# Performance work log

Hardware: AMD Instinct MI355X
Metric: run time of the kernel (lower is better)

Reference implementation:

```python
import jax, jax.numpy as jnp
import numpy as np
from jax import lax

B, N, D_FEAT = 16, 4096, 20
NPOINT, NSAMPLE = 1024, 32
MLP = [64, 64, 128]
IN_CH = 3 + 1 + D_FEAT  # grouped_xyz_norm(3) + L2 norm(1) + grouped_depth_norm(20)
BN_EPS = 1e-5


def setup_inputs() -> dict:
    key = jax.random.key(0)
    ks = jax.random.split(key, 20)
    inp = {
        "xyz": jax.random.normal(ks[0], (B, 3, N), dtype=jnp.float32),
        "feature": jax.random.normal(ks[1], (B, N, D_FEAT), dtype=jnp.float32),
    }
    last = IN_CH
    kidx = 2
    for li, out_ch in enumerate(MLP):
        inp[f"w{li}"] = jax.random.normal(ks[kidx], (out_ch, last), dtype=jnp.float32) * (1.0 / np.sqrt(last)); kidx += 1
        inp[f"b{li}"] = jax.random.normal(ks[kidx], (out_ch,), dtype=jnp.float32) * 0.01; kidx += 1
        inp[f"g{li}"] = 1.0 + 0.1 * jax.random.normal(ks[kidx], (out_ch,), dtype=jnp.float32); kidx += 1
        inp[f"bt{li}"] = 0.1 * jax.random.normal(ks[kidx], (out_ch,), dtype=jnp.float32); kidx += 1
        last = out_ch
    return inp


def square_distance(src, dst):
    # [B,S,C] x [B,M,C] -> [B,S,M]
    d = -2.0 * jnp.einsum("bsc,bmc->bsm", src, dst)
    d = d + jnp.sum(src * src, -1)[:, :, None]
    d = d + jnp.sum(dst * dst, -1)[:, None, :]
    return d


def farthest_point_sample(pts, npoint):
    # pts: [B,N,C]; deterministic start at index 0 (torch uses random start)
    b, n, _ = pts.shape
    bidx = jnp.arange(b)

    def step(carry, _):
        dist, far = carry
        centroid = pts[bidx, far]                      # [B,C]
        d = jnp.sum((pts - centroid[:, None, :]) ** 2, -1)  # [B,N]
        dist = jnp.minimum(dist, d)
        nxt = jnp.argmax(dist, -1)
        return (dist, nxt), far

    init = (jnp.full((b, n), 1e10, pts.dtype), jnp.zeros((b,), jnp.int32))
    _, idx = lax.scan(step, init, None, length=npoint)
    return idx.T  # [B,npoint]


def _gather_groups(points, idx):
    # points [B,N,C], idx [B,S,K] -> [B,S,K,C]
    return jax.vmap(lambda p, i: p[i])(points, idx)


def conv_bn_relu(x, w, b, g, bt):
    # x [B,C,K,S]; 1x1 conv = channel matmul; BN in training mode (batch stats, biased var)
    y = jnp.einsum("bcks,oc->boks", x, w) + b[None, :, None, None]
    mu = jnp.mean(y, axis=(0, 2, 3), keepdims=True)
    var = jnp.mean((y - mu) ** 2, axis=(0, 2, 3), keepdims=True)
    y = (y - mu) * lax.rsqrt(var + BN_EPS)
    y = y * g[None, :, None, None] + bt[None, :, None, None]
    return jax.nn.relu(y)


def reference(xyz, feature, w0, b0, g0, bt0, w1, b1, g1, bt1, w2, b2, g2, bt2):
    xyz_n = jnp.transpose(xyz, (0, 2, 1))              # [B,N,3]
    combined = jnp.concatenate([xyz_n, feature], -1)   # [B,N,23]
    fps_idx = farthest_point_sample(combined, NPOINT)  # [B,S]

    new_bin = jnp.take_along_axis(feature, fps_idx[:, :, None], axis=1)  # [B,S,20]
    new_xyz = jnp.take_along_axis(xyz_n, fps_idx[:, :, None], axis=1)    # [B,S,3]

    sqd = square_distance(new_bin, feature) + square_distance(new_xyz, xyz_n)  # [B,S,N]
    idx = jnp.argsort(sqd, axis=-1)[:, :, :NSAMPLE]    # [B,S,K]

    gxyz = _gather_groups(xyz_n, idx)                  # [B,S,K,3]
    gfeat = _gather_groups(feature, idx)               # [B,S,K,20]
    gxyz_norm = gxyz - new_xyz[:, :, None, :]
    gdep_norm = gfeat - new_bin[:, :, None, :]
    nrm = jnp.sqrt(jnp.maximum(jnp.sum(gxyz_norm ** 2, -1, keepdims=True), 1e-12))
    new_points = jnp.concatenate([gxyz_norm, nrm, gdep_norm], -1)  # [B,S,K,24]

    x = jnp.transpose(new_points, (0, 3, 2, 1))        # [B,24,K,S]
    for (w, b, g, bt) in [(w0, b0, g0, bt0), (w1, b1, g1, bt1), (w2, b2, g2, bt2)]:
        x = conv_bn_relu(x, w, b, g, bt)
    out = jnp.max(x, axis=2)                           # [B,128,S]
    return jnp.transpose(new_xyz, (0, 2, 1)), out, new_bin
```

## Files before the change

### kernel.cpp

```cpp
#include <hip/hip_runtime.h>

#define BB 16
#define NN 4096
#define DFEAT 20
#define SS 1024
#define KK 32
#define MM (BB*SS*KK)

#define WS_STATS   0ull
#define WS_PARAMS  8192ull
#define WS_FPSIDX  12288ull
#define WS_CENT    81920ull
#define WS_KNN     1654784ull
#define WS_COMB    3751936ull
#define WS_YB      10043392ull
#define WS_NEED    77152256ull

typedef float v2f __attribute__((ext_vector_type(2)));

static __device__ __forceinline__ unsigned short f2bf(float f){
    unsigned u = __float_as_uint(f);
    unsigned r = (u + 0x7FFFu + ((u >> 16) & 1u)) >> 16;
    return (unsigned short)r;
}
static __device__ __forceinline__ float bf2f(unsigned short v){
    return __uint_as_float((unsigned)v << 16);
}
static __device__ __forceinline__ void pinv2(v2f& x){
    asm volatile("" : "+v"(x));
}

static __device__ __forceinline__ unsigned long long max64(unsigned long long a, unsigned long long b){
    return a > b ? a : b;
}
template<int CTRL>
static __device__ __forceinline__ unsigned dpp32_or0(unsigned x){
    return (unsigned)__builtin_amdgcn_update_dpp(0, (int)x, CTRL, 0xf, 0xf, true);
}
template<int CTRL>
static __device__ __forceinline__ unsigned long long dpp_move64(unsigned long long k){
    int tlo = __builtin_amdgcn_update_dpp(0, (int)(unsigned)k,         CTRL, 0xf, 0xf, true);
    int thi = __builtin_amdgcn_update_dpp(0, (int)(unsigned)(k >> 32), CTRL, 0xf, 0xf, true);
    return ((unsigned long long)(unsigned)thi << 32) | (unsigned)tlo;
}
static __device__ __forceinline__ unsigned umax32(unsigned a, unsigned b){
    return a > b ? a : b;
}
static __device__ __forceinline__ unsigned wave_max_u32(unsigned x){
    x = umax32(x, dpp32_or0<0x111>(x));
    x = umax32(x, dpp32_or0<0x112>(x));
    x = umax32(x, dpp32_or0<0x114>(x));
    x = umax32(x, dpp32_or0<0x118>(x));
    x = umax32(x, dpp32_or0<0x142>(x));
    x = umax32(x, dpp32_or0<0x143>(x));
    return x;
}

__global__ void k_zstats(double* __restrict__ stats){
    int t = threadIdx.x;
#pragma unroll
    for (int i = 0; i < 4; ++i) stats[i*256 + t] = 0.0;
}

__global__ void k_fail(float* __restrict__ out, int n){
    int i = blockIdx.x * 256 + threadIdx.x;
    if (i < n) out[i] = 0.f;
}

__global__ __launch_bounds__(256) void k_build(const float* __restrict__ xyz,
                                               const float* __restrict__ feat,
                                               float* __restrict__ comb)
{
    int idx = blockIdx.x * 256 + threadIdx.x;
    int b = idx >> 12, j = idx & 4095;
    float c[24];
    c[0] = xyz[((size_t)b*3 + 0)*NN + j];
    c[1] = xyz[((size_t)b*3 + 1)*NN + j];
    c[2] = xyz[((size_t)b*3 + 2)*NN + j];
    const float* f = feat + ((size_t)b*NN + j)*DFEAT;
#pragma unroll
    for (int d = 0; d < 20; ++d) c[3+d] = f[d];
    c[23] = 0.f;
    float* out = comb + (size_t)idx * 24;
#pragma unroll
    for (int q = 0; q < 6; ++q)
        ((float4*)out)[q] = make_float4(c[4*q], c[4*q+1], c[4*q+2], c[4*q+3]);
}

__global__ __launch_bounds__(1024, 4) void k_fps(const float* __restrict__ comb,
                                                 int* __restrict__ fpsidx)
{
    int b = blockIdx.x, t = threadIdx.x;
    const float* C = comb + (size_t)b * NN * 24;
    v2f pt2[2][24];
    v2f dist2[2];
#pragma unroll
    for (int p = 0; p < 4; ++p){
        const float4* r = (const float4*)(C + (size_t)(t + 1024*p) * 24);
#pragma unroll
        for (int q = 0; q < 6; ++q){
            float4 v = r[q];
            pt2[p>>1][4*q+0][p&1] = v.x;
            pt2[p>>1][4*q+1][p&1] = v.y;
            pt2[p>>1][4*q+2][p&1] = v.z;
            pt2[p>>1][4*q+3][p&1] = v.w;
        }
    }
#pragma unroll
    for (int k = 0; k < 2; ++k)
        dist2[k] = (v2f){1e10f, 1e10f};

    __shared__ __align__(16) unsigned long long wkey[2][16];
    __shared__ __align__(16) float wpt[2][16][24];
    __shared__ int fps_lds[SS];
    int lane = t & 63, w = t >> 6;
    unsigned nt = 0xFFFFFFFFu - (unsigned)t;
    int far = 0;

    float cc[24];
    {
        const float4* crow = (const float4*)C;
#pragma unroll
        for (int q = 0; q < 6; ++q){
            float4 cv = crow[q];
            cc[4*q] = cv.x; cc[4*q+1] = cv.y; cc[4*q+2] = cv.z; cc[4*q+3] = cv.w;
        }
    }

    for (int s = 0; s < SS; ++s){
#pragma unroll
        for (int k = 0; k < 2; ++k)
#pragma unroll
            for (int q = 0; q < 23; ++q) pinv2(pt2[k][q]);

        if (t == 0) fps_lds[s] = far;
        v2f acc2[2];
#pragma unroll
        for (int k = 0; k < 2; ++k){
            v2f d0 = pt2[k][0] - cc[0];
            acc2[k] = d0 * d0;
        }
#pragma unroll
        for (int q = 1; q < 23; ++q){
            float cq = cc[q];
#pragma unroll
            for (int k = 0; k < 2; ++k){
                v2f dd = pt2[k][q] - cq;
                acc2[k] = __builtin_elementwise_fma(dd, dd, acc2[k]);
            }
        }
#pragma unroll
        for (int k = 0; k < 2; ++k)
            dist2[k] = __builtin_elementwise_min(dist2[k], acc2[k]);
        v2f mt = __builtin_elementwise_max(dist2[0], dist2[1]);
        float mf = fmaxf(mt[0], mt[1]);
        unsigned maxbits = __float_as_uint(mf);
        int pstar = 0;
#pragma unroll
        for (int p = 3; p >= 0; --p)
            if (__float_as_uint(dist2[p>>1][p&1]) == maxbits) pstar = p;

        unsigned M = __builtin_amdgcn_readlane((int)wave_max_u32(maxbits), 63);
        unsigned cidx = (maxbits == M) ? (nt - ((unsigned)pstar << 10)) : 0u;
        unsigned widxc = __builtin_amdgcn_readlane((int)wave_max_u32(cidx), 63);
        unsigned widx  = 0xFFFFFFFFu - widxc;

        int par = s & 1;
        if (lane == 63)
            wkey[par][w] = ((unsigned long long)M << 32) | (unsigned long long)widxc;
        if (t == (int)(widx & 1023u)){
            int pw = (int)(widx >> 10);
            float* dst = wpt[par][w];
            switch (pw){
#define PE(P,q) pt2[(P)>>1][q][(P)&1]
#define STASH(P) case P: \
                ((float4*)dst)[0] = make_float4(PE(P,0),PE(P,1),PE(P,2),PE(P,3)); \
                ((float4*)dst)[1] = make_float4(PE(P,4),PE(P,5),PE(P,6),PE(P,7)); \
                ((float4*)dst)[2] = make_float4(PE(P,8),PE(P,9),PE(P,10),PE(P,11)); \
                ((float4*)dst)[3] = make_float4(PE(P,12),PE(P,13),PE(P,14),PE(P,15)); \
                ((float4*)dst)[4] = make_float4(PE(P,16),PE(P,17),PE(P,18),PE(P,19)); \
                ((float4*)dst)[5] = make_float4(PE(P,20),PE(P,21),PE(P,22),0.f); \
                break;
            STASH(0) STASH(1) STASH(2) STASH(3)
#undef STASH
#undef PE
            }
        }
        __syncthreads();
        unsigned long long k2 = wkey[par][lane & 15];
        k2 = max64(k2, dpp_move64<0x121>(k2));
        k2 = max64(k2, dpp_move64<0x122>(k2));
        k2 = max64(k2, dpp_move64<0x124>(k2));
        k2 = max64(k2, dpp_move64<0x128>(k2));
        far = (int)(0xFFFFFFFFu - (unsigned)(k2 & 0xFFFFFFFFull));
        int wg = (far & 1023) >> 6;
        const float4* crow = (const float4*)wpt[par][wg];
#pragma unroll
        for (int q = 0; q < 6; ++q){
            float4 cv = crow[q];
            cc[4*q] = cv.x; cc[4*q+1] = cv.y; cc[4*q+2] = cv.z; cc[4*q+3] = cv.w;
        }
    }
    __syncthreads();
    fpsidx[b*SS + t] = fps_lds[t];
}

__global__ __launch_bounds__(256) void k_gather(const float* __restrict__ comb,
                                                const int* __restrict__ fpsidx,
                                                float* __restrict__ cent,
                                                float* __restrict__ out0,
                                                float* __restrict__ out2)
{
    int idx = blockIdx.x * 256 + threadIdx.x;
    int b = idx >> 10, s = idx & 1023;
    int j = fpsidx[idx];
    const float* row = comb + ((size_t)b*NN + j) * 24;
    float* cr = cent + (size_t)idx * 24;
#pragma unroll
    for (int q = 0; q < 6; ++q) ((float4*)cr)[q] = ((const float4*)row)[q];
#pragma unroll
    for (int c = 0; c < 3; ++c) out0[((size_t)b*3 + c)*SS + s] = row[c];
    float* o2 = out2 + (size_t)idx * 20;
#pragma unroll
    for (int d = 0; d < 20; ++d) o2[d] = row[3 + d];
}

__global__ __launch_bounds__(256) void k_knn(const float* __restrict__ comb,
                                             const float* __restrict__ cent,
                                             int* __restrict__ knn)
{
    int w = threadIdx.x >> 6, lane = threadIdx.x & 63;
    int r = blockIdx.x * 4 + w;
    int b = r >> 10;
    const float* crow = cent + (size_t)r * 24;
    const float* P0 = comb + (size_t)b * NN * 24;
    double cc[24];
#pragma unroll
    for (int q = 0; q < 24; ++q) cc[q] = (double)crow[q];
    unsigned u[64];
#pragma unroll
    for (int k = 0; k < 64; ++k){
        int j = k*64 + lane;
        const float4* pr = (const float4*)(P0 + (size_t)j * 24);
        double acc = 0.0;
#pragma unroll
        for (int q = 0; q < 6; ++q){
            float4 v = pr[q];
            double d0 = (double)v.x - cc[4*q];
            double d1 = (double)v.y - cc[4*q+1];
            double d2 = (double)v.z - cc[4*q+2];
            double d3 = (double)v.w - cc[4*q+3];
            acc += d0*d0; acc += d1*d1; acc += d2*d2; acc += d3*d3;
        }
        u[k] = __float_as_uint((float)acc);
    }
    unsigned lo = 0u, hi = 0xFFFFFFFFu;
    for (int it = 0; it < 32; ++it){
        unsigned mid = lo + ((hi - lo) >> 1);
        int cnt = 0;
#pragma unroll
        for (int k = 0; k < 64; ++k) cnt += (u[k] <= mid) ? 1 : 0;
#pragma unroll
        for (int off = 32; off > 0; off >>= 1) cnt += __shfl_xor(cnt, off);
        if (cnt >= KK) hi = mid; else lo = mid + 1;
    }
    unsigned T = lo;
    int* orow = knn + (size_t)r * KK;
    unsigned long long lmask = (1ull << lane) - 1ull;
    int pos = 0;
#pragma unroll
    for (int k = 0; k < 64; ++k){
        bool lt = (u[k] < T);
        unsigned long long mk = __ballot(lt);
        if (lt) orow[pos + __popcll(mk & lmask)] = k*64 + lane;
        pos += __popcll(mk);
    }
#pragma unroll
    for (int k = 0; k < 64; ++k){
        if (pos >= KK) break;
        bool eq = (u[k] == T);
        unsigned long long mk = __ballot(eq);
        int rk = __popcll(mk & lmask);
        if (eq && (pos + rk) < KK) orow[pos + rk] = k*64 + lane;
        pos += __popcll(mk);
    }
}

__global__ __launch_bounds__(256) void k_l1(const float* __restrict__ comb,
                                            const float* __restrict__ cent,
                                            const int* __restrict__ knn,
                                            const float* __restrict__ w0,
                                            const float* __restrict__ b0,
                                            unsigned short* __restrict__ yb)
{
    __shared__ float Wt[24][64];
    __shared__ float Xt[24][68];
    int t = threadIdx.x;
    int m_base = blockIdx.x * 64;
    for (int i = t; i < 1536; i += 256){
        int o = i / 24, c = i - o*24;
        Wt[c][o] = w0[i];
    }
    {
        int sm = t & 63, g = t >> 6;
        int m = m_base + sm;
        int b = m >> 15;
        int row = m >> 5;
        int j = knn[m];
        const float* P  = comb + ((size_t)b*NN + j) * 24;
        const float* Cc = cent + (size_t)row * 24;
        if (g == 0){
            float dx = P[0]-Cc[0], dy = P[1]-Cc[1], dz = P[2]-Cc[2];
            Xt[0][sm] = dx; Xt[1][sm] = dy; Xt[2][sm] = dz;
            float n2 = dx*dx; n2 = fmaf(dy, dy, n2); n2 = fmaf(dz, dz, n2);
            Xt[3][sm] = sqrtf(fmaxf(n2, 1e-12f));
            Xt[4][sm] = P[3] - Cc[3];
            Xt[5][sm] = P[4] - Cc[4];
        } else {
#pragma unroll
            for (int cq = 0; cq < 6; ++cq){
                int c = 6*g + cq;
                Xt[c][sm] = P[c-1] - Cc[c-1];
            }
        }
    }
    __syncthreads();
    int i = t >> 4, jj = t & 15;
    float acc[4][4] = {};
#pragma unroll
    for (int c = 0; c < 24; ++c){
        float4 wv = *(const float4*)&Wt[c][i*4];
        float4 xv = *(const float4*)&Xt[c][jj*4];
        float wr[4] = {wv.x, wv.y, wv.z, wv.w};
        float xr[4] = {xv.x, xv.y, xv.z, xv.w};
#pragma unroll
        for (int a = 0; a < 4; ++a)
#pragma unroll
            for (int q = 0; q < 4; ++q) acc[a][q] = fmaf(wr[a], xr[q], acc[a][q]);
    }
#pragma unroll
    for (int oi = 0; oi < 4; ++oi){
        int o = i*4 + oi;
        float bb = b0[o];
        ushort4 rv;
        rv.x = f2bf(acc[oi][0]+bb); rv.y = f2bf(acc[oi][1]+bb);
        rv.z = f2bf(acc[oi][2]+bb); rv.w = f2bf(acc[oi][3]+bb);
        *(ushort4*)&yb[(size_t)o*MM + m_base + jj*4] = rv;
    }
}

__global__ __launch_bounds__(256) void k_stats(const unsigned short* __restrict__ y,
                                               double* __restrict__ stats)
{
    const int chunks = 8;
    int c = blockIdx.x / chunks, ch = blockIdx.x % chunks;
    size_t base = (size_t)c * MM + (size_t)ch * (MM / chunks);
    double s1 = 0.0, s2 = 0.0;
    const unsigned short* p = y + base;
    for (int i = threadIdx.x; i < MM/chunks; i += 256){
        float v = bf2f(p[i]);
        s1 += v; s2 += (double)v * v;
    }
#pragma unroll
    for (int off = 32; off > 0; off >>= 1){
        s1 += __shfl_xor(s1, off);
        s2 += __shfl_xor(s2, off);
    }
    __shared__ double ps1[4], ps2[4];
    int w = threadIdx.x >> 6, lane = threadIdx.x & 63;
    if (lane == 0){ ps1[w] = s1; ps2[w] = s2; }
    __syncthreads();
    if (threadIdx.x == 0){
        atomicAdd(&stats[c*2 + 0], ps1[0]+ps1[1]+ps1[2]+ps1[3]);
        atomicAdd(&stats[c*2 + 1], ps2[0]+ps2[1]+ps2[2]+ps2[3]);
    }
}

__global__ void k_affine(const double* __restrict__ stats, float* __restrict__ params, int C)
{
    int c = threadIdx.x;
    if (c < C){
        double mu = stats[c*2] / (double)MM;
        double var = stats[c*2 + 1] / (double)MM - mu*mu;
        params[c*2 + 0] = (float)mu;
        params[c*2 + 1] = (float)(1.0 / sqrt(var + 1e-5));
    }
}

__global__ __launch_bounds__(256) void k_l2(unsigned short* __restrict__ yb,
                                            const float* __restrict__ prm,
                                            const float* __restrict__ gg,
                                            const float* __restrict__ bt,
                                            const float* __restrict__ w,
                                            const float* __restrict__ bias)
{
    __shared__ float Wt[64][64];
    __shared__ float Xt[64][68];
    int t = threadIdx.x;
    int m_base = blockIdx.x * 64;
    for (int i = t; i < 4096; i += 256){
        int o = i >> 6, c = i & 63;
        Wt[c][o] = w[i];
    }
#pragma unroll
    for (int rp = 0; rp < 16; ++rp){
        int idx = rp*256 + t;
        int c = idx >> 6, mm2 = idx & 63;
        float v = bf2f(yb[(size_t)c*MM + m_base + mm2]);
        float t1 = (v - prm[c*2]) * prm[c*2 + 1];
        Xt[c][mm2] = fmaxf(fmaf(t1, gg[c], bt[c]), 0.f);
    }
    __syncthreads();
    int i = t >> 4, jj = t & 15;
    float acc[4][4] = {};
#pragma unroll
    for (int c = 0; c < 64; ++c){
        float4 wv = *(const float4*)&Wt[c][i*4];
        float4 xv = *(const float4*)&Xt[c][jj*4];
        float wr[4] = {wv.x, wv.y, wv.z, wv.w};
        float xr[4] = {xv.x, xv.y, xv.z, xv.w};
#pragma unroll
        for (int a = 0; a < 4; ++a)
#pragma unroll
            for (int q = 0; q < 4; ++q) acc[a][q] = fmaf(wr[a], xr[q], acc[a][q]);
    }
#pragma unroll
    for (int oi = 0; oi < 4; ++oi){
        int o = i*4 + oi;
        float bb = bias[o];
        ushort4 rv;
        rv.x = f2bf(acc[oi][0]+bb); rv.y = f2bf(acc[oi][1]+bb);
        rv.z = f2bf(acc[oi][2]+bb); rv.w = f2bf(acc[oi][3]+bb);
        *(ushort4*)&yb[(size_t)o*MM + m_base + jj*4] = rv;
    }
}

__global__ __launch_bounds__(256) void k_l3s(const unsigned short* __restrict__ yb,
                                             const float* __restrict__ prm,
                                             const float* __restrict__ gg,
                                             const float* __restrict__ bt,
                                             const float* __restrict__ w,
                                             const float* __restrict__ bias,
                                             double* __restrict__ stats)
{
    __shared__ float Wt[64][128];
    __shared__ float Xt[64][68];
    int t = threadIdx.x;
    for (int i = t; i < 8192; i += 256){
        int o = i >> 6, c = i & 63;
        Wt[c][o] = w[i];
    }
    int i = t >> 4, jj = t & 15;
    double s1[8] = {}, s2[8] = {};
    for (int tt = 0; tt < 16; ++tt){
        int m_base = (blockIdx.x * 16 + tt) * 64;
        __syncthreads();
#pragma unroll
        for (int rp = 0; rp < 16; ++rp){
            int idx = rp*256 + t;
            int c = idx >> 6, mm2 = idx & 63;
            float v = bf2f(yb[(size_t)c*MM + m_base + mm2]);
            float t1 = (v - prm[c*2]) * prm[c*2 + 1];
            Xt[c][mm2] = fmaxf(fmaf(t1, gg[c], bt[c]), 0.f);
        }
        __syncthreads();
        float acc[8][4] = {};
#pragma unroll
        for (int c = 0; c < 64; ++c){
            float4 w0v = *(const float4*)&Wt[c][i*8];
            float4 w1v = *(const float4*)&Wt[c][i*8 + 4];
            float4 xv  = *(const float4*)&Xt[c][jj*4];
            float wr[8] = {w0v.x, w0v.y, w0v.z, w0v.w, w1v.x, w1v.y, w1v.z, w1v.w};
            float xr[4] = {xv.x, xv.y, xv.z, xv.w};
#pragma unroll
            for (int a = 0; a < 8; ++a)
#pragma unroll
                for (int q = 0; q < 4; ++q) acc[a][q] = fmaf(wr[a], xr[q], acc[a][q]);
        }
#pragma unroll
        for (int oi = 0; oi < 8; ++oi){
            float bb = bias[i*8 + oi];
#pragma unroll
            for (int q = 0; q < 4; ++q){
                float v = acc[oi][q] + bb;
                s1[oi] += v;
                s2[oi] += (double)v * v;
            }
        }
    }
#pragma unroll
    for (int oi = 0; oi < 8; ++oi){
#pragma unroll
        for (int off = 1; off < 16; off <<= 1){
            s1[oi] += __shfl_xor(s1[oi], off);
            s2[oi] += __shfl_xor(s2[oi], off);
        }
    }
    if (jj == 0){
#pragma unroll
        for (int oi = 0; oi < 8; ++oi){
            int o = i*8 + oi;
            atomicAdd(&stats[o*2 + 0], s1[oi]);
            atomicAdd(&stats[o*2 + 1], s2[oi]);
        }
    }
}

__global__ __launch_bounds__(256) void k_final(const unsigned short* __restrict__ yb,
                                               const float* __restrict__ prm2,
                                               const float* __restrict__ g1c,
                                               const float* __restrict__ bt1c,
                                               const float* __restrict__ w,
                                               const float* __restrict__ bias,
                                               const float* __restrict__ prm3,
                                               const float* __restrict__ g2c,
                                               const float* __restrict__ bt2c,
                                               float* __restrict__ out1)
{
    __shared__ float Wt[64][128];
    __shared__ float Xt[64][68];
    int t = threadIdx.x;
    int m_base = blockIdx.x * 64;
    for (int i = t; i < 8192; i += 256){
        int o = i >> 6, c = i & 63;
        Wt[c][o] = w[i];
    }
#pragma unroll
    for (int rp = 0; rp < 16; ++rp){
        int idx = rp*256 + t;
        int c = idx >> 6, mm2 = idx & 63;
        float v = bf2f(yb[(size_t)c*MM + m_base + mm2]);
        float t1 = (v - prm2[c*2]) * prm2[c*2 + 1];
        Xt[c][mm2] = fmaxf(fmaf(t1, g1c[c], bt1c[c]), 0.f);
    }
    __syncthreads();
    int i = t >> 4, jj = t & 15;
    float acc[8][4] = {};
#pragma unroll
    for (int c = 0; c < 64; ++c){
        float4 w0v = *(const float4*)&Wt[c][i*8];
        float4 w1v = *(const float4*)&Wt[c][i*8 + 4];
        float4 xv  = *(const float4*)&Xt[c][jj*4];
        float wr[8] = {w0v.x, w0v.y, w0v.z, w0v.w, w1v.x, w1v.y, w1v.z, w1v.w};
        float xr[4] = {xv.x, xv.y, xv.z, xv.w};
#pragma unroll
        for (int a = 0; a < 8; ++a)
#pragma unroll
            for (int q = 0; q < 4; ++q) acc[a][q] = fmaf(wr[a], xr[q], acc[a][q]);
    }
    float mx[8];
#pragma unroll
    for (int oi = 0; oi < 8; ++oi){
        int o = i*8 + oi;
        float bb = bias[o];
        float mu = prm3[o*2], inv = prm3[o*2 + 1], gv = g2c[o], bv = bt2c[o];
        float m = 0.f;
#pragma unroll
        for (int q = 0; q < 4; ++q){
            float v = acc[oi][q] + bb;
            float r = fmaxf(fmaf((v - mu) * inv, gv, bv), 0.f);
            m = fmaxf(m, r);
        }
        mx[oi] = m;
    }
#pragma unroll
    for (int oi = 0; oi < 8; ++oi){
#pragma unroll
        for (int off = 1; off < 8; off <<= 1)
            mx[oi] = fmaxf(mx[oi], __shfl_xor(mx[oi], off));
    }
    if ((jj & 7) == 0){
        int rg = (m_base >> 5) + (jj >> 3);
        int b = rg >> 10, s = rg & 1023;
#pragma unroll
        for (int oi = 0; oi < 8; ++oi)
            out1[(size_t)b*131072 + (size_t)(i*8 + oi)*1024 + s] = mx[oi];
    }
}

extern "C" void kernel_launch(void* const* d_in, const int* in_sizes, int n_in,
                              void* d_out, int out_size, void* d_ws, size_t ws_size,
                              hipStream_t stream)
{
    const float* xyz  = (const float*)d_in[0];
    const float* feat = (const float*)d_in[1];
    const float* w0 = (const float*)d_in[2];  const float* b0  = (const float*)d_in[3];
    const float* g0 = (const float*)d_in[4];  const float* bt0 = (const float*)d_in[5];
    const float* w1 = (const float*)d_in[6];  const float* b1  = (const float*)d_in[7];
    const float* g1 = (const float*)d_in[8];  const float* bt1 = (const float*)d_in[9];
    const float* w2 = (const float*)d_in[10]; const float* b2  = (const float*)d_in[11];
    const float* g2 = (const float*)d_in[12]; const float* bt2 = (const float*)d_in[13];

    float* out0 = (float*)d_out;
    float* out1 = (float*)d_out + 49152;
    float* out2 = (float*)d_out + 49152 + 2097152;

    if (ws_size < WS_NEED){
        k_fail<<<(out_size + 255)/256, 256, 0, stream>>>((float*)d_out, out_size);
        return;
    }

    char* ws = (char*)d_ws;
    double* stats = (double*)(ws + WS_STATS);
    float* params = (float*)(ws + WS_PARAMS);
    int*   fpsidx = (int*)(ws + WS_FPSIDX);
    float* cent   = (float*)(ws + WS_CENT);
    int*   knn    = (int*)(ws + WS_KNN);
    float* comb   = (float*)(ws + WS_COMB);
    unsigned short* yb = (unsigned short*)(ws + WS_YB);

    k_zstats<<<1,    256, 0, stream>>>(stats);
    k_build <<<256,  256, 0, stream>>>(xyz, feat, comb);
    k_fps   <<<16,  1024, 0, stream>>>(comb, fpsidx);
    k_gather<<<64,   256, 0, stream>>>(comb, fpsidx, cent, out0, out2);
    k_knn   <<<4096, 256, 0, stream>>>(comb, cent, knn);
    k_l1    <<<8192, 256, 0, stream>>>(comb, cent, knn, w0, b0, yb);
    k_stats <<<512,  256, 0, stream>>>(yb, stats);
    k_affine<<<1,    128, 0, stream>>>(stats, params, 64);
    k_l2    <<<8192, 256, 0, stream>>>(yb, params, g0, bt0, w1, b1);
    k_stats <<<512,  256, 0, stream>>>(yb, stats + 256);
    k_affine<<<1,    128, 0, stream>>>(stats + 256, params + 256, 64);
    k_l3s   <<<512,  256, 0, stream>>>(yb, params + 256, g1, bt1, w2, b2, stats + 512);
    k_affine<<<1,    128, 0, stream>>>(stats + 512, params + 512, 128);
    k_final <<<8192, 256, 0, stream>>>(yb, params + 256, g1, bt1, w2, b2,
                                       params + 512, g2, bt2, out1);
}
```

Baseline: 3.256 ms.

## Stream FPS point data from global memory each iteration instead of registers

The FPS kernel no longer keeps its four points per thread resident in packed v2f registers. It reloads them from global/L2 every iteration, using an opaque zero offset so the compiler cannot hoist the loads out of the loop. The winning centroid is now read straight from global memory by index, which removes the per-wave LDS stash of the candidate point. This lowers register pressure and drops the stash branch, at the cost of about 96 KB of reloads per block per iteration, scalar instead of packed FMA math, and a dependent global load on the serial critical path.

```diff
diff --git a/kernel.cpp b/kernel.cpp
--- a/kernel.cpp
+++ b/kernel.cpp
@@ -16,8 +16,6 @@
 #define WS_YB      10043392ull
 #define WS_NEED    77152256ull
 
-typedef float v2f __attribute__((ext_vector_type(2)));
-
 static __device__ __forceinline__ unsigned short f2bf(float f){
     unsigned u = __float_as_uint(f);
     unsigned r = (u + 0x7FFFu + ((u >> 16) & 1u)) >> 16;
@@ -25,9 +23,6 @@
 }
 static __device__ __forceinline__ float bf2f(unsigned short v){
     return __uint_as_float((unsigned)v << 16);
-}
-static __device__ __forceinline__ void pinv2(v2f& x){
-    asm volatile("" : "+v"(x));
 }
 
 static __device__ __forceinline__ unsigned long long max64(unsigned long long a, unsigned long long b){
@@ -92,31 +87,18 @@
 {
     int b = blockIdx.x, t = threadIdx.x;
     const float* C = comb + (size_t)b * NN * 24;
-    v2f pt2[2][24];
-    v2f dist2[2];
-#pragma unroll
-    for (int p = 0; p < 4; ++p){
-        const float4* r = (const float4*)(C + (size_t)(t + 1024*p) * 24);
-#pragma unroll
-        for (int q = 0; q < 6; ++q){
-            float4 v = r[q];
-            pt2[p>>1][4*q+0][p&1] = v.x;
-            pt2[p>>1][4*q+1][p&1] = v.y;
-            pt2[p>>1][4*q+2][p&1] = v.z;
-            pt2[p>>1][4*q+3][p&1] = v.w;
-        }
-    }
-#pragma unroll
-    for (int k = 0; k < 2; ++k)
-        dist2[k] = (v2f){1e10f, 1e10f};
+    float dist[4] = {1e10f, 1e10f, 1e10f, 1e10f};
 
     __shared__ __align__(16) unsigned long long wkey[2][16];
-    __shared__ __align__(16) float wpt[2][16][24];
     __shared__ int fps_lds[SS];
     int lane = t & 63, w = t >> 6;
     unsigned nt = 0xFFFFFFFFu - (unsigned)t;
     int far = 0;
 
+    size_t poff[4];
+#pragma unroll
+    for (int p = 0; p < 4; ++p) poff[p] = (size_t)(t + 1024*p) * 24;
+
     float cc[24];
     {
         const float4* crow = (const float4*)C;
@@ -128,64 +110,53 @@
     }
 
     for (int s = 0; s < SS; ++s){
-#pragma unroll
-        for (int k = 0; k < 2; ++k)
-#pragma unroll
-            for (int q = 0; q < 23; ++q) pinv2(pt2[k][q]);
-
         if (t == 0) fps_lds[s] = far;
-        v2f acc2[2];
-#pragma unroll
-        for (int k = 0; k < 2; ++k){
-            v2f d0 = pt2[k][0] - cc[0];
-            acc2[k] = d0 * d0;
-        }
-#pragma unroll
-        for (int q = 1; q < 23; ++q){
-            float cq = cc[q];
-#pragma unroll
-            for (int k = 0; k < 2; ++k){
-                v2f dd = pt2[k][q] - cq;
-                acc2[k] = __builtin_elementwise_fma(dd, dd, acc2[k]);
+        size_t zz = 0;
+        asm volatile("" : "+s"(zz));
+        const float* Cl = C + zz;
+
+#pragma unroll
+        for (int g = 0; g < 2; ++g){
+            const float4* pa = (const float4*)(Cl + poff[2*g + 0]);
+            const float4* pb = (const float4*)(Cl + poff[2*g + 1]);
+            float4 ra0 = pa[0], ra1 = pa[1], ra2 = pa[2], ra3 = pa[3], ra4 = pa[4], ra5 = pa[5];
+            float4 rb0 = pb[0], rb1 = pb[1], rb2 = pb[2], rb3 = pb[3], rb4 = pb[4], rb5 = pb[5];
+            float A[24] = {ra0.x,ra0.y,ra0.z,ra0.w, ra1.x,ra1.y,ra1.z,ra1.w,
+                           ra2.x,ra2.y,ra2.z,ra2.w, ra3.x,ra3.y,ra3.z,ra3.w,
+                           ra4.x,ra4.y,ra4.z,ra4.w, ra5.x,ra5.y,ra5.z,ra5.w};
+            float Bv[24] = {rb0.x,rb0.y,rb0.z,rb0.w, rb1.x,rb1.y,rb1.z,rb1.w,
+                            rb2.x,rb2.y,rb2.z,rb2.w, rb3.x,rb3.y,rb3.z,rb3.w,
+                            rb4.x,rb4.y,rb4.z,rb4.w, rb5.x,rb5.y,rb5.z,rb5.w};
+            float da = A[0]  - cc[0];
+            float db = Bv[0] - cc[0];
+            float sa = da * da;
+            float sb = db * db;
+#pragma unroll
+            for (int q = 1; q < 23; ++q){
+                float xa = A[q]  - cc[q];
+                sa = fmaf(xa, xa, sa);
+                float xb = Bv[q] - cc[q];
+                sb = fmaf(xb, xb, sb);
             }
-        }
-#pragma unroll
-        for (int k = 0; k < 2; ++k)
-            dist2[k] = __builtin_elementwise_min(dist2[k], acc2[k]);
-        v2f mt = __builtin_elementwise_max(dist2[0], dist2[1]);
-        float mf = fmaxf(mt[0], mt[1]);
+            dist[2*g + 0] = fminf(dist[2*g + 0], sa);
+            dist[2*g + 1] = fminf(dist[2*g + 1], sb);
+        }
+        float m01 = fmaxf(dist[0], dist[1]);
+        float m23 = fmaxf(dist[2], dist[3]);
+        float mf  = fmaxf(m01, m23);
         unsigned maxbits = __float_as_uint(mf);
         int pstar = 0;
 #pragma unroll
         for (int p = 3; p >= 0; --p)
-            if (__float_as_uint(dist2[p>>1][p&1]) == maxbits) pstar = p;
+            if (__float_as_uint(dist[p]) == maxbits) pstar = p;
 
         unsigned M = __builtin_amdgcn_readlane((int)wave_max_u32(maxbits), 63);
         unsigned cidx = (maxbits == M) ? (nt - ((unsigned)pstar << 10)) : 0u;
         unsigned widxc = __builtin_amdgcn_readlane((int)wave_max_u32(cidx), 63);
-        unsigned widx  = 0xFFFFFFFFu - widxc;
 
         int par = s & 1;
         if (lane == 63)
             wkey[par][w] = ((unsigned long long)M << 32) | (unsigned long long)widxc;
-        if (t == (int)(widx & 1023u)){
-            int pw = (int)(widx >> 10);
-            float* dst = wpt[par][w];
-            switch (pw){
-#define PE(P,q) pt2[(P)>>1][q][(P)&1]
-#define STASH(P) case P: \
-                ((float4*)dst)[0] = make_float4(PE(P,0),PE(P,1),PE(P,2),PE(P,3)); \
-                ((float4*)dst)[1] = make_float4(PE(P,4),PE(P,5),PE(P,6),PE(P,7)); \
-                ((float4*)dst)[2] = make_float4(PE(P,8),PE(P,9),PE(P,10),PE(P,11)); \
-                ((float4*)dst)[3] = make_float4(PE(P,12),PE(P,13),PE(P,14),PE(P,15)); \
-                ((float4*)dst)[4] = make_float4(PE(P,16),PE(P,17),PE(P,18),PE(P,19)); \
-                ((float4*)dst)[5] = make_float4(PE(P,20),PE(P,21),PE(P,22),0.f); \
-                break;
-            STASH(0) STASH(1) STASH(2) STASH(3)
-#undef STASH
-#undef PE
-            }
-        }
         __syncthreads();
         unsigned long long k2 = wkey[par][lane & 15];
         k2 = max64(k2, dpp_move64<0x121>(k2));
@@ -193,8 +164,7 @@
         k2 = max64(k2, dpp_move64<0x124>(k2));
         k2 = max64(k2, dpp_move64<0x128>(k2));
         far = (int)(0xFFFFFFFFu - (unsigned)(k2 & 0xFFFFFFFFull));
-        int wg = (far & 1023) >> 6;
-        const float4* crow = (const float4*)wpt[par][wg];
+        const float4* crow = (const float4*)(C + (size_t)far * 24);
 #pragma unroll
         for (int q = 0; q < 6; ++q){
             float4 cv = crow[q];
```

Measured after the change: 6.262 ms. 92.3% more time.
